# Performance work log

Hardware: AMD Instinct MI355X
Metric: run time of the kernel (lower is better)

## Reference

```python
import jax, jax.numpy as jnp
import numpy as np

B, T = 128, 160000

def setup_inputs() -> dict:
    key = jax.random.key(0)
    waveform = jax.random.normal(key, (B, T), dtype=jnp.float32)
    return {"waveform": waveform}

def reference(waveform):
    # waveform: [B, T]. Normalize to ~[0,1] then delta-sigma PDM encode.
    x = waveform / 2 + 0.5
    def step(err, xt):          # err: [B], xt: [B]
        err = err + xt
        s = (err > 0).astype(x.dtype)
        return err - s, s
    init = jnp.zeros(x.shape[0], dtype=x.dtype)
    _, spikes_t = jax.lax.scan(step, init, x.T)  # [T, B]
    return spikes_t.T                            # [B, T]
```

## Files before the change

kernel.cpp:

```cpp
#include <hip/hip_runtime.h>


#define T_LEN 160000
#define CHUNK 64
#define NV (CHUNK / 4)

__device__ __forceinline__ void pdm_step(float v, float& e, float& o) {
    float x = v * 0.5f + 0.5f;
    float u = e + x;
    bool sp = u > 0.0f;
    o = sp ? 1.0f : 0.0f;
    e = sp ? (u - 1.0f) : u;
}

__device__ __forceinline__ void pdm_chunk(float4* buf, float& e) {
    #pragma unroll
    for (int i = 0; i < NV; ++i) {
        float4 v = buf[i];
        float r0, r1, r2, r3;
        pdm_step(v.x, e, r0);
        pdm_step(v.y, e, r1);
        pdm_step(v.z, e, r2);
        pdm_step(v.w, e, r3);
        buf[i] = make_float4(r0, r1, r2, r3);
    }
}

__global__ __launch_bounds__(64, 1)
void pdm_encode(const float* __restrict__ w, float* __restrict__ out, int nRows) {
    int row = blockIdx.x * blockDim.x + threadIdx.x;
    if (row >= nRows) return;

    const float4* __restrict__ src = reinterpret_cast<const float4*>(w + (size_t)row * T_LEN);
    float4* __restrict__ dst = reinterpret_cast<float4*>(out + (size_t)row * T_LEN);

    const int NC = T_LEN / CHUNK;

    float4 A[NV], Bb[NV];

    #pragma unroll
    for (int i = 0; i < NV; ++i) A[i] = src[i];

    float e = 0.0f;

    for (int k = 0; k < NC / 2; ++k) {
        const int c0 = 2 * k;
        const int c1 = c0 + 1;

        #pragma unroll
        for (int i = 0; i < NV; ++i) Bb[i] = src[(size_t)c1 * NV + i];

        pdm_chunk(A, e);
        #pragma unroll
        for (int i = 0; i < NV; ++i) dst[(size_t)c0 * NV + i] = A[i];

        if (k + 1 < NC / 2) {
            #pragma unroll
            for (int i = 0; i < NV; ++i) A[i] = src[(size_t)(c0 + 2) * NV + i];
        }

        pdm_chunk(Bb, e);
        #pragma unroll
        for (int i = 0; i < NV; ++i) dst[(size_t)c1 * NV + i] = Bb[i];
    }
}

extern "C" void kernel_launch(void* const* d_in, const int* in_sizes, int n_in,
                              void* d_out, int out_size, void* d_ws, size_t ws_size,
                              hipStream_t stream) {
    const float* w = (const float*)d_in[0];
    float* out = (float*)d_out;

    const int nRows = in_sizes[0] / T_LEN;
    const int block = 64;
    const int grid = (nRows + block - 1) / block;

    pdm_encode<<<grid, block, 0, stream>>>(w, out, nRows);
}
```

Before: 3.428 ms.

## Stage input chunks through LDS with async global_load_lds triple buffering

Replaces the register double-buffered global loads with direct global-to-LDS async loads (global_load_lds) into a three-deep LDS ring, then reads each chunk back with ds_read_b128. The aim is to keep more loads in flight per lane and cut the register pressure and load latency exposed on the serial error-feedback chain. The cost is explicit vmcnt(0) and lgkmcnt(0) waits every chunk, which may serialize load issue. It also relies on hand-written inline asm and sched barriers that the compiler cannot reorder.

Result: slower. 3.664 ms (+6.9%).

```diff
diff --git a/kernel.cpp b/kernel.cpp
--- a/kernel.cpp
+++ b/kernel.cpp
@@ -3,7 +3,20 @@
 
 #define T_LEN 160000
 #define CHUNK 64
-#define NV (CHUNK / 4)
+#define NPC 16
+#define NC (T_LEN / CHUNK)
+#define BUFB (NPC * 64 * 16)
+
+typedef float f32x4 __attribute__((ext_vector_type(4)));
+#define AS1 __attribute__((address_space(1)))
+#define AS3 __attribute__((address_space(3)))
+
+#define SB() __builtin_amdgcn_sched_barrier(0)
+#define DRAIN_VM() do { asm volatile("s_waitcnt vmcnt(0)" ::: "memory"); SB(); } while (0)
+#define DRAIN_LGKM() do { asm volatile("s_waitcnt lgkmcnt(0)" ::: "memory"); SB(); } while (0)
+
+#define DSREAD(dst, addr, OFF) \
+    asm volatile("ds_read_b128 %0, %1 offset:" #OFF : "=v"(dst) : "v"(addr))
 
 __device__ __forceinline__ void pdm_step(float v, float& e, float& o) {
     float x = v * 0.5f + 0.5f;
@@ -13,56 +26,81 @@
     e = sp ? (u - 1.0f) : u;
 }
 
-__device__ __forceinline__ void pdm_chunk(float4* buf, float& e) {
-    #pragma unroll
-    for (int i = 0; i < NV; ++i) {
-        float4 v = buf[i];
-        float r0, r1, r2, r3;
-        pdm_step(v.x, e, r0);
-        pdm_step(v.y, e, r1);
-        pdm_step(v.z, e, r2);
-        pdm_step(v.w, e, r3);
-        buf[i] = make_float4(r0, r1, r2, r3);
-    }
+__device__ __forceinline__ f32x4 pdm_piece(f32x4 v, float& e) {
+    float r0, r1, r2, r3;
+    pdm_step(v[0], e, r0);
+    pdm_step(v[1], e, r1);
+    pdm_step(v[2], e, r2);
+    pdm_step(v[3], e, r3);
+    f32x4 r; r[0] = r0; r[1] = r1; r[2] = r2; r[3] = r3;
+    return r;
 }
 
 __global__ __launch_bounds__(64, 1)
 void pdm_encode(const float* __restrict__ w, float* __restrict__ out, int nRows) {
-    int row = blockIdx.x * blockDim.x + threadIdx.x;
+    __shared__ float lds[3][NPC][64][4];
+
+    const int lane = threadIdx.x;
+    const int row = blockIdx.x * 64 + lane;
     if (row >= nRows) return;
 
-    const float4* __restrict__ src = reinterpret_cast<const float4*>(w + (size_t)row * T_LEN);
-    float4* __restrict__ dst = reinterpret_cast<float4*>(out + (size_t)row * T_LEN);
+    const float* src = w + (size_t)row * T_LEN;
+    float* dst = out + (size_t)row * T_LEN;
 
-    const int NC = T_LEN / CHUNK;
+    const unsigned lds0 = (unsigned)(uintptr_t)(AS3 float*)&lds[0][0][0][0];
+    const unsigned myoff = lds0 + (unsigned)lane * 16u;
 
-    float4 A[NV], Bb[NV];
+    #define DMA(b_, c_) do {                                               \
+        const float* _g = src + (size_t)(c_) * CHUNK;                      \
+        _Pragma("unroll")                                                  \
+        for (int j = 0; j < NPC; ++j)                                      \
+            __builtin_amdgcn_global_load_lds(                              \
+                (const AS1 void*)(_g + j * 4),                             \
+                (AS3 void*)&lds[b_][j][0][0], 16, 0, 0);                   \
+    } while (0)
 
-    #pragma unroll
-    for (int i = 0; i < NV; ++i) A[i] = src[i];
+    DMA(0, 0); DMA(1, 1); DMA(2, 2);
 
     float e = 0.0f;
 
-    for (int k = 0; k < NC / 2; ++k) {
-        const int c0 = 2 * k;
-        const int c1 = c0 + 1;
+    for (int c = 0; c < NC; ++c) {
+        const int b = c % 3;
+        const unsigned boff = myoff + (unsigned)b * BUFB;
 
-        #pragma unroll
-        for (int i = 0; i < NV; ++i) Bb[i] = src[(size_t)c1 * NV + i];
+        DRAIN_VM();
 
-        pdm_chunk(A, e);
-        #pragma unroll
-        for (int i = 0; i < NV; ++i) dst[(size_t)c0 * NV + i] = A[i];
+        f32x4 v0,v1,v2,v3,v4,v5,v6,v7,v8,v9,v10,v11,v12,v13,v14,v15;
+        DSREAD(v0,  boff, 0);     DSREAD(v1,  boff, 1024);
+        DSREAD(v2,  boff, 2048);  DSREAD(v3,  boff, 3072);
+        DSREAD(v4,  boff, 4096);  DSREAD(v5,  boff, 5120);
+        DSREAD(v6,  boff, 6144);  DSREAD(v7,  boff, 7168);
+        DSREAD(v8,  boff, 8192);  DSREAD(v9,  boff, 9216);
+        DSREAD(v10, boff, 10240); DSREAD(v11, boff, 11264);
+        DSREAD(v12, boff, 12288); DSREAD(v13, boff, 13312);
+        DSREAD(v14, boff, 14336); DSREAD(v15, boff, 15360);
+        DRAIN_LGKM();
 
-        if (k + 1 < NC / 2) {
-            #pragma unroll
-            for (int i = 0; i < NV; ++i) A[i] = src[(size_t)(c0 + 2) * NV + i];
-        }
+        if (c < NC - 3) DMA(b, c + 3);
 
-        pdm_chunk(Bb, e);
-        #pragma unroll
-        for (int i = 0; i < NV; ++i) dst[(size_t)c1 * NV + i] = Bb[i];
+        float* dc = dst + (size_t)c * CHUNK;
+        *(f32x4*)(dc +  0) = pdm_piece(v0,  e);
+        *(f32x4*)(dc +  4) = pdm_piece(v1,  e);
+        *(f32x4*)(dc +  8) = pdm_piece(v2,  e);
+        *(f32x4*)(dc + 12) = pdm_piece(v3,  e);
+        *(f32x4*)(dc + 16) = pdm_piece(v4,  e);
+        *(f32x4*)(dc + 20) = pdm_piece(v5,  e);
+        *(f32x4*)(dc + 24) = pdm_piece(v6,  e);
+        *(f32x4*)(dc + 28) = pdm_piece(v7,  e);
+        *(f32x4*)(dc + 32) = pdm_piece(v8,  e);
+        *(f32x4*)(dc + 36) = pdm_piece(v9,  e);
+        *(f32x4*)(dc + 40) = pdm_piece(v10, e);
+        *(f32x4*)(dc + 44) = pdm_piece(v11, e);
+        *(f32x4*)(dc + 48) = pdm_piece(v12, e);
+        *(f32x4*)(dc + 52) = pdm_piece(v13, e);
+        *(f32x4*)(dc + 56) = pdm_piece(v14, e);
+        *(f32x4*)(dc + 60) = pdm_piece(v15, e);
     }
+    #undef DMA
 }
 
 extern "C" void kernel_launch(void* const* d_in, const int* in_sizes, int n_in,
```
